# Kernel tuning notes

Hardware: AMD Instinct MI355X
Metric: run time of the kernel (lower is better)

Reference implementation:

```python
import jax, jax.numpy as jnp
import numpy as np

B, T, IN, EH, GH = 256, 512, 128, 512, 512  # batch, time, channels, enc hidden, gen hidden
UPDATE_BIAS = 1.0
CLIP_VAL = 5.0


def setup_inputs() -> dict:
    key = jax.random.key(0)
    ks = jax.random.split(key, 7)
    s = 0.05  # weight scale to keep gates unsaturated
    return {
        "src": jax.random.normal(ks[0], (B, T, IN), jnp.float32),
        "eps": jax.random.normal(ks[1], (B, GH), jnp.float32),  # reparam noise for generator IC
        "enc_Wi": jax.random.normal(ks[2], (3 * EH, IN), jnp.float32) * s,   # torch GRU weight_ih_l0 (r,z,n)
        "enc_Wh": jax.random.normal(ks[3], (3 * EH, EH), jnp.float32) * s,   # torch GRU weight_hh_l0
        "enc2gen_W": jax.random.normal(ks[4], (2 * GH, EH), jnp.float32) * s,  # Linear enc_state -> ic params
        "gen_Wh_ru": jax.random.normal(ks[5], (2 * GH, GH), jnp.float32) * s,  # GruCellModified fc_h_ru
        "gen_W_rhc": jax.random.normal(ks[6], (GH, GH), jnp.float32) * s,      # GruCellModified fc_rh_c
    }


def _forward(src, eps, enc_Wi, enc_Wh, enc2gen_W, gen_Wh_ru, gen_W_rhc):
    b, t, _ = src.shape
    H = enc_Wh.shape[1]
    # ---- encoder: standard GRU (bias=False), batch_first, 1 layer, unidirectional ----
    xW = jnp.einsum('bti,ki->tbk', src, enc_Wi)  # [T,B,3H], input projections hoisted out of scan

    def enc_step(h, xw):
        gh = h @ enc_Wh.T  # [B,3H]
        xr, xz, xn = jnp.split(xw, 3, axis=-1)
        hr, hz, hn = jnp.split(gh, 3, axis=-1)
        r = jax.nn.sigmoid(xr + hr)
        z = jax.nn.sigmoid(xz + hz)
        n = jnp.tanh(xn + r * hn)
        h_new = (1.0 - z) * n + z * h
        return h_new, None

    h0 = jnp.zeros((b, H), src.dtype)
    enc_last, _ = jax.lax.scan(enc_step, h0, xW)  # [B,EH]

    # ---- enc2gen Linear -> generator IC distribution params ----
    ic_params = enc_last @ enc2gen_W.T  # [B, 2*GH]
    mu, lv = jnp.split(ic_params, 2, axis=1)
    ic = mu + jnp.exp(0.5 * lv) * eps  # reparameterized sample, [B,GH]

    # ---- generator: GruCellModified recurrence, input_size=0 (no input term) ----
    def gen_step(h, _):
        ru = h @ gen_Wh_ru.T  # [B,2*GH]
        r, u = jnp.split(ru, 2, axis=-1)
        r = jax.nn.sigmoid(r)
        u = jax.nn.sigmoid(u + UPDATE_BIAS)  # forced update-gate bias
        c = jnp.tanh((r * h) @ gen_W_rhc.T)
        h_new = u * h + (1.0 - u) * c
        return h_new, h_new

    _, gen_hidden = jax.lax.scan(gen_step, ic, None, length=t)  # [T,B,GH]
    gen_out = jnp.clip(gen_hidden.transpose(1, 0, 2), -CLIP_VAL, CLIP_VAL)  # [B,T,GH]
    return gen_out, ic_params


def reference(src, eps, enc_Wi, enc_Wh, enc2gen_W, gen_Wh_ru, gen_W_rhc):
    return _forward(src, eps, enc_Wi, enc_Wh, enc2gen_W, gen_Wh_ru, gen_W_rhc)
```

## Files before the change

### kernel.cpp

```cpp
#include <hip/hip_runtime.h>
#include <hip/hip_bf16.h>
#include <math.h>

#define BB 256
#define TT 512
#define INW 128
#define EH 512
#define GH 512

#define NGRP 16
#define NGB 16
#define MG 16
#define NB 32
#define FLS 16

typedef __attribute__((ext_vector_type(8))) short bf16x8;
typedef __attribute__((ext_vector_type(4))) float f32x4;
typedef __attribute__((ext_vector_type(2))) unsigned long long u64x2;

__device__ __forceinline__ float sigm(float x){ return 1.0f/(1.0f+__expf(-x)); }
__device__ __forceinline__ short f2bf(float x){
    __hip_bfloat16 h = __float2bfloat16(x);
    return *reinterpret_cast<short*>(&h);
}

__device__ __forceinline__ unsigned long long ld_coh64(const unsigned long long* p){
    return __hip_atomic_load(p, __ATOMIC_RELAXED, __HIP_MEMORY_SCOPE_AGENT);
}
__device__ __forceinline__ void st_coh32(unsigned* p, unsigned v){
    __hip_atomic_store(p, v, __ATOMIC_RELAXED, __HIP_MEMORY_SCOPE_AGENT);
}

__device__ __forceinline__ void grp_barrier(unsigned* gf, int ng, unsigned e){
    asm volatile("s_waitcnt vmcnt(0)" ::: "memory");
    __syncthreads();
    if (threadIdx.x == 0) st_coh32(gf + ng*FLS, e);
    if (threadIdx.x < 64) {
        const unsigned* p = gf + (threadIdx.x & (NGB-1)) * FLS;
        long spins = 0;
        for (;;) {
            unsigned v = __hip_atomic_load(p, __ATOMIC_RELAXED, __HIP_MEMORY_SCOPE_AGENT);
            if (__all((int)(v >= e))) break;
            if (++spins > (1L << 20)) break;
        }
    }
    __syncthreads();
}

__device__ __forceinline__ void pack_store_bf(unsigned* dst_even, short bv, int l15){
    unsigned mine = (unsigned short)bv;
    unsigned othr = __shfl_xor(mine, 1);
    if (!(l15 & 1)) st_coh32(dst_even, (othr << 16) | mine);
}

__global__ __launch_bounds__(512, 1) void enc_kernel(
    const float* __restrict__ src,
    const float* __restrict__ Wi,
    const float* __restrict__ Wh,
    short*       __restrict__ hbf,
    float*       __restrict__ hencf,
    unsigned*    __restrict__ flags)
{
    __shared__ __align__(16) char sH[MG*1024];
    __shared__ __align__(16) char sX[MG*256];
    __shared__ float sR[MG*33];
    __shared__ float sZ[MG*33];
    __shared__ float sHfp[MG*33];

    const int bid = blockIdx.x;
    const int g = bid >> 4, ng = bid & 15;
    const int tid = threadIdx.x;
    const int wid = tid >> 6, lane = tid & 63;
    const int l15 = lane & 15, lk = lane >> 4;
    const int j0 = ng * NB;
    const int b0 = g * MG;
    unsigned* gf = flags + g * NGB * FLS;

    bf16x8 whB[16], wxB[4];
    const int gate = wid >> 1, ct = wid & 1;
    const int col = ct*16 + l15;
    if (wid < 6) {
        const float* wrh = Wh + (size_t)(gate*EH + j0 + col) * EH;
        const float* wrx = Wi + (size_t)(gate*EH + j0 + col) * INW;
        #pragma unroll
        for (int kt = 0; kt < 16; ++kt) {
            int ke = kt*32 + lk*8;
            float4 f0 = *(const float4*)(wrh + ke);
            float4 f1 = *(const float4*)(wrh + ke + 4);
            bf16x8 v;
            v[0]=f2bf(f0.x); v[1]=f2bf(f0.y); v[2]=f2bf(f0.z); v[3]=f2bf(f0.w);
            v[4]=f2bf(f1.x); v[5]=f2bf(f1.y); v[6]=f2bf(f1.z); v[7]=f2bf(f1.w);
            whB[kt] = v;
        }
        #pragma unroll
        for (int kt = 0; kt < 4; ++kt) {
            int ke = kt*32 + lk*8;
            float4 f0 = *(const float4*)(wrx + ke);
            float4 f1 = *(const float4*)(wrx + ke + 4);
            bf16x8 v;
            v[0]=f2bf(f0.x); v[1]=f2bf(f0.y); v[2]=f2bf(f0.z); v[3]=f2bf(f0.w);
            v[4]=f2bf(f1.x); v[5]=f2bf(f1.y); v[6]=f2bf(f1.z); v[7]=f2bf(f1.w);
            wxB[kt] = v;
        }
    }
    sHfp[(tid >> 5)*33 + (tid & 31)] = 0.0f;

    for (int t = 0; t < TT; ++t) {
        const short* hsrc = hbf + (size_t)(t & 1) * BB * EH;
        short*       hdst = hbf + (size_t)((t + 1) & 1) * BB * EH;

        #pragma unroll
        for (int i = 0; i < 2; ++i) {
            int c = i*512 + tid;
            int row = c >> 6;
            int kb  = (c & 63) << 4;
            const unsigned long long* gp =
                (const unsigned long long*)((const char*)(hsrc + (size_t)(b0 + row)*EH) + kb);
            unsigned long long v0 = ld_coh64(gp);
            unsigned long long v1 = ld_coh64(gp + 1);
            u64x2 v; v[0] = v0; v[1] = v1;
            *(u64x2*)(sH + row*1024 + (kb ^ ((row & 7) << 4))) = v;
        }
        if (tid < 256) {
            int row = tid >> 4, k = (tid & 15) * 8;
            const float* sp = src + ((size_t)(b0 + row)*TT + t)*INW + k;
            float4 f0 = *(const float4*)sp;
            float4 f1 = *(const float4*)(sp + 4);
            bf16x8 v;
            v[0]=f2bf(f0.x); v[1]=f2bf(f0.y); v[2]=f2bf(f0.z); v[3]=f2bf(f0.w);
            v[4]=f2bf(f1.x); v[5]=f2bf(f1.y); v[6]=f2bf(f1.z); v[7]=f2bf(f1.w);
            *(bf16x8*)(sX + row*256 + ((k*2) ^ ((row & 7) << 4))) = v;
        }
        __syncthreads();

        f32x4 acc0 = {0.f,0.f,0.f,0.f}, acc1 = {0.f,0.f,0.f,0.f};
        f32x4 accx = {0.f,0.f,0.f,0.f};
        if (wid < 6) {
            const int asw = (l15 & 7) << 4;
            const char* hb = sH + l15*1024;
            const char* xb = sX + l15*256;
            #pragma unroll
            for (int kt = 0; kt < 8; ++kt) {
                int kb = kt*64 + lk*16;
                bf16x8 a = *(const bf16x8*)(hb + (kb ^ asw));
                acc0 = __builtin_amdgcn_mfma_f32_16x16x32_bf16(a, whB[kt], acc0, 0, 0, 0);
            }
            #pragma unroll
            for (int kt = 8; kt < 16; ++kt) {
                int kb = kt*64 + lk*16;
                bf16x8 a = *(const bf16x8*)(hb + (kb ^ asw));
                acc1 = __builtin_amdgcn_mfma_f32_16x16x32_bf16(a, whB[kt], acc1, 0, 0, 0);
            }
            #pragma unroll
            for (int kt = 0; kt < 4; ++kt) {
                int kb = kt*64 + lk*16;
                bf16x8 a = *(const bf16x8*)(xb + (kb ^ asw));
                accx = __builtin_amdgcn_mfma_f32_16x16x32_bf16(a, wxB[kt], accx, 0, 0, 0);
            }
        }
        f32x4 acch = acc0 + acc1;
        if (wid < 2) {
            #pragma unroll
            for (int v = 0; v < 4; ++v)
                sR[(lk*4 + v)*33 + col] = sigm(accx[v] + acch[v]);
        } else if (wid < 4) {
            #pragma unroll
            for (int v = 0; v < 4; ++v)
                sZ[(lk*4 + v)*33 + col] = sigm(accx[v] + acch[v]);
        }
        __syncthreads();
        if (wid == 4 || wid == 5) {
            #pragma unroll
            for (int v = 0; v < 4; ++v) {
                int row = lk*4 + v;
                float r  = sR[row*33 + col];
                float z  = sZ[row*33 + col];
                float n  = tanhf(accx[v] + r * acch[v]);
                float hp = sHfp[row*33 + col];
                float hn = (1.f - z)*n + z*hp;
                sHfp[row*33 + col] = hn;
                unsigned* dst = (unsigned*)&hdst[(size_t)(b0 + row)*EH + j0 + ct*16 + (l15 & ~1)];
                pack_store_bf(dst, f2bf(hn), l15);
                if (t == TT - 1) hencf[(size_t)(b0 + row)*EH + j0 + col] = hn;
            }
        }
        grp_barrier(gf, ng, (unsigned)(t + 1));
    }
}

__global__ __launch_bounds__(256) void ic_kernel(
    const float* __restrict__ henc,
    const float* __restrict__ W,
    const float* __restrict__ eps,
    float*       __restrict__ out_icp,
    float*       __restrict__ gh0f,
    short*       __restrict__ gh0b)
{
    __shared__ float hb[EH];
    const int b = blockIdx.x, tid = threadIdx.x;
    for (int k = tid; k < EH; k += 256) hb[k] = henc[(size_t)b*EH + k];
    __syncthreads();

    for (int jj = tid; jj < GH; jj += 256) {
        const float4* wm = (const float4*)(W + (size_t)jj * EH);
        const float4* wl = (const float4*)(W + (size_t)(GH + jj) * EH);
        float am = 0.f, al = 0.f;
        #pragma unroll 4
        for (int k4 = 0; k4 < EH/4; ++k4) {
            float4 h = ((const float4*)hb)[k4];
            float4 a = wm[k4], c = wl[k4];
            am += h.x*a.x + h.y*a.y + h.z*a.z + h.w*a.w;
            al += h.x*c.x + h.y*c.y + h.z*c.z + h.w*c.w;
        }
        out_icp[(size_t)b*2*GH + jj]      = am;
        out_icp[(size_t)b*2*GH + GH + jj] = al;
        float icv = am + __expf(0.5f * al) * eps[(size_t)b*GH + jj];
        gh0f[(size_t)b*GH + jj] = icv;
        gh0b[(size_t)b*GH + jj] = f2bf(icv);
    }
}

__global__ __launch_bounds__(512, 1) void gen_kernel(
    const float* __restrict__ Wru,
    const float* __restrict__ Wc,
    const float* __restrict__ gh0f,
    short*       __restrict__ hbf,
    short*       __restrict__ rhbf,
    float*       __restrict__ out,
    unsigned*    __restrict__ flags)
{
    __shared__ __align__(16) char sH[MG*1024];
    __shared__ float sU[MG*33];
    __shared__ float sHfp[MG*33];

    const int bid = blockIdx.x;
    const int g = bid >> 4, ng = bid & 15;
    const int tid = threadIdx.x;
    const int wid = tid >> 6, lane = tid & 63;
    const int l15 = lane & 15, lk = lane >> 4;
    const int j0 = ng * NB;
    const int b0 = g * MG;
    unsigned* gf = flags + g * NGB * FLS;
    short* rhg = rhbf + (size_t)g * MG * GH;

    bf16x8 wB[16];
    const int gate = wid >> 1, ct = wid & 1;
    const int col = ct*16 + l15;
    if (wid < 6) {
        const float* wr;
        if (gate == 0)      wr = Wru + (size_t)(j0 + col) * GH;
        else if (gate == 1) wr = Wru + (size_t)(GH + j0 + col) * GH;
        else                wr = Wc  + (size_t)(j0 + col) * GH;
        #pragma unroll
        for (int kt = 0; kt < 16; ++kt) {
            int ke = kt*32 + lk*8;
            float4 f0 = *(const float4*)(wr + ke);
            float4 f1 = *(const float4*)(wr + ke + 4);
            bf16x8 v;
            v[0]=f2bf(f0.x); v[1]=f2bf(f0.y); v[2]=f2bf(f0.z); v[3]=f2bf(f0.w);
            v[4]=f2bf(f1.x); v[5]=f2bf(f1.y); v[6]=f2bf(f1.z); v[7]=f2bf(f1.w);
            wB[kt] = v;
        }
    }
    {
        int row = tid >> 5, c = tid & 31;
        sHfp[row*33 + c] = gh0f[(size_t)(b0 + row)*GH + j0 + c];
    }

    for (int t = 0; t < TT; ++t) {
        const short* hsrc = hbf + (size_t)(t & 1) * BB * GH;
        short*       hdst = hbf + (size_t)((t + 1) & 1) * BB * GH;

        #pragma unroll
        for (int i = 0; i < 2; ++i) {
            int c = i*512 + tid;
            int row = c >> 6;
            int kb  = (c & 63) << 4;
            const unsigned long long* gp =
                (const unsigned long long*)((const char*)(hsrc + (size_t)(b0 + row)*GH) + kb);
            unsigned long long v0 = ld_coh64(gp);
            unsigned long long v1 = ld_coh64(gp + 1);
            u64x2 v; v[0] = v0; v[1] = v1;
            *(u64x2*)(sH + row*1024 + (kb ^ ((row & 7) << 4))) = v;
        }
        __syncthreads();

        if (wid < 4) {
            const int asw = (l15 & 7) << 4;
            const char* hb = sH + l15*1024;
            f32x4 acc0 = {0.f,0.f,0.f,0.f}, acc1 = {0.f,0.f,0.f,0.f};
            #pragma unroll
            for (int kt = 0; kt < 8; ++kt) {
                int kb = kt*64 + lk*16;
                bf16x8 a = *(const bf16x8*)(hb + (kb ^ asw));
                acc0 = __builtin_amdgcn_mfma_f32_16x16x32_bf16(a, wB[kt], acc0, 0, 0, 0);
            }
            #pragma unroll
            for (int kt = 8; kt < 16; ++kt) {
                int kb = kt*64 + lk*16;
                bf16x8 a = *(const bf16x8*)(hb + (kb ^ asw));
                acc1 = __builtin_amdgcn_mfma_f32_16x16x32_bf16(a, wB[kt], acc1, 0, 0, 0);
            }
            f32x4 acc = acc0 + acc1;
            if (wid < 2) {
                #pragma unroll
                for (int v = 0; v < 4; ++v) {
                    int row = lk*4 + v;
                    float hp = sHfp[row*33 + col];
                    float rv = sigm(acc[v]);
                    unsigned* dst = (unsigned*)&rhg[(size_t)row*GH + j0 + ct*16 + (l15 & ~1)];
                    pack_store_bf(dst, f2bf(rv * hp), l15);
                }
            } else {
                #pragma unroll
                for (int v = 0; v < 4; ++v)
                    sU[(lk*4 + v)*33 + col] = sigm(acc[v] + 1.0f);
            }
        }
        grp_barrier(gf, ng, (unsigned)(2*t + 1));

        #pragma unroll
        for (int i = 0; i < 2; ++i) {
            int c = i*512 + tid;
            int row = c >> 6;
            int kb  = (c & 63) << 4;
            const unsigned long long* gp =
                (const unsigned long long*)((const char*)(rhg + (size_t)row*GH) + kb);
            unsigned long long v0 = ld_coh64(gp);
            unsigned long long v1 = ld_coh64(gp + 1);
            u64x2 v; v[0] = v0; v[1] = v1;
            *(u64x2*)(sH + row*1024 + (kb ^ ((row & 7) << 4))) = v;
        }
        __syncthreads();

        if (wid == 4 || wid == 5) {
            const int asw = (l15 & 7) << 4;
            const char* hb = sH + l15*1024;
            f32x4 acc0 = {0.f,0.f,0.f,0.f}, acc1 = {0.f,0.f,0.f,0.f};
            #pragma unroll
            for (int kt = 0; kt < 8; ++kt) {
                int kb = kt*64 + lk*16;
                bf16x8 a = *(const bf16x8*)(hb + (kb ^ asw));
                acc0 = __builtin_amdgcn_mfma_f32_16x16x32_bf16(a, wB[kt], acc0, 0, 0, 0);
            }
            #pragma unroll
            for (int kt = 8; kt < 16; ++kt) {
                int kb = kt*64 + lk*16;
                bf16x8 a = *(const bf16x8*)(hb + (kb ^ asw));
                acc1 = __builtin_amdgcn_mfma_f32_16x16x32_bf16(a, wB[kt], acc1, 0, 0, 0);
            }
            f32x4 acc = acc0 + acc1;
            #pragma unroll
            for (int v = 0; v < 4; ++v) {
                int row = lk*4 + v;
                float cv = tanhf(acc[v]);
                float u  = sU[row*33 + col];
                float hp = sHfp[row*33 + col];
                float hn = u*hp + (1.0f - u)*cv;
                sHfp[row*33 + col] = hn;
                unsigned* dst = (unsigned*)&hdst[(size_t)(b0 + row)*GH + j0 + ct*16 + (l15 & ~1)];
                pack_store_bf(dst, f2bf(hn), l15);
                out[((size_t)(b0 + row)*TT + t)*GH + j0 + col] = fminf(fmaxf(hn, -5.0f), 5.0f);
            }
        }
        grp_barrier(gf, ng, (unsigned)(2*t + 2));
    }
}

extern "C" void kernel_launch(void* const* d_in, const int* in_sizes, int n_in,
                              void* d_out, int out_size, void* d_ws, size_t ws_size,
                              hipStream_t stream) {
    (void)in_sizes; (void)n_in; (void)out_size; (void)ws_size;

    const float* src    = (const float*)d_in[0];
    const float* eps    = (const float*)d_in[1];
    const float* enc_Wi = (const float*)d_in[2];
    const float* enc_Wh = (const float*)d_in[3];
    const float* e2g    = (const float*)d_in[4];
    const float* gWru   = (const float*)d_in[5];
    const float* gWc    = (const float*)d_in[6];
    float* out = (float*)d_out;

    char* ws = (char*)d_ws;
    unsigned* encFl = (unsigned*)ws;
    unsigned* genFl = (unsigned*)(ws + 16384);
    float* hencf = (float*)(ws + 32768);
    float* gh0f  = (float*)(ws + 32768 + 512*1024);
    short* encH  = (short*)(ws + 32768 + 1024*1024);
    short* genH  = (short*)(ws + 32768 + 1536*1024);
    short* rhbf  = (short*)(ws + 32768 + 2048*1024);

    hipMemsetAsync(ws, 0, 32768, stream);
    hipMemsetAsync(encH, 0, (size_t)BB*EH*2, stream);

    enc_kernel<<<dim3(256), dim3(512), 0, stream>>>(src, enc_Wi, enc_Wh, encH, hencf, encFl);
    ic_kernel <<<dim3(256), dim3(256), 0, stream>>>(hencf, e2g, eps,
                                                    out + (size_t)BB*TT*GH, gh0f, genH);
    gen_kernel<<<dim3(256), dim3(512), 0, stream>>>(gWru, gWc, gh0f, genH, rhbf, out,
                                                    genFl);
}
```

Before: 4.905 ms.

## Split each block's batch tile into two half-groups and ping-pong their recurrence steps

Each workgroup now owns two independent 8-row batch sub-groups with separate flag sets and double-buffered shared tiles. It alternates compute between them, so the group-barrier wait and global staging loads of one half overlap with the MFMA work of the other. Hidden-state loads for the next half are issued right after polling and written to LDS later, which hides load latency behind compute. In exchange, half of each 16-row MFMA tile is wasted, there are twice as many flag polls per step, and the synchronisation pattern is more complex and fragile.

```diff
diff --git a/kernel.cpp b/kernel.cpp
--- a/kernel.cpp
+++ b/kernel.cpp
@@ -8,9 +8,8 @@
 #define EH 512
 #define GH 512
 
-#define NGRP 16
 #define NGB 16
-#define MG 16
+#define MGH 8
 #define NB 32
 #define FLS 16
 
@@ -30,15 +29,23 @@
 __device__ __forceinline__ void st_coh32(unsigned* p, unsigned v){
     __hip_atomic_store(p, v, __ATOMIC_RELAXED, __HIP_MEMORY_SCOPE_AGENT);
 }
-
-__device__ __forceinline__ void grp_barrier(unsigned* gf, int ng, unsigned e){
-    asm volatile("s_waitcnt vmcnt(0)" ::: "memory");
-    __syncthreads();
-    if (threadIdx.x == 0) st_coh32(gf + ng*FLS, e);
-    if (threadIdx.x < 64) {
-        const unsigned* p = gf + (threadIdx.x & (NGB-1)) * FLS;
+__device__ __forceinline__ void wait_vm0(){ asm volatile("s_waitcnt vmcnt(0)" ::: "memory"); }
+
+struct Stg { unsigned long long q0, q1; };
+__device__ __forceinline__ Stg stage_issue(const short* rowbase, int kb){
+    const unsigned long long* gp = (const unsigned long long*)((const char*)rowbase + kb);
+    Stg s; s.q0 = ld_coh64(gp); s.q1 = ld_coh64(gp + 1); return s;
+}
+__device__ __forceinline__ void stage_write(char* sbuf, int row, int kb, Stg s){
+    u64x2 v; v[0] = s.q0; v[1] = s.q1;
+    *(u64x2*)(sbuf + row*1024 + (kb ^ (row << 4))) = v;
+}
+
+__device__ __forceinline__ void poll16(const unsigned* fl, unsigned e){
+    if (threadIdx.x < 64){
+        const unsigned* p = fl + (threadIdx.x & (NGB-1)) * FLS;
         long spins = 0;
-        for (;;) {
+        for(;;){
             unsigned v = __hip_atomic_load(p, __ATOMIC_RELAXED, __HIP_MEMORY_SCOPE_AGENT);
             if (__all((int)(v >= e))) break;
             if (++spins > (1L << 20)) break;
@@ -47,10 +54,143 @@
     __syncthreads();
 }
 
-__device__ __forceinline__ void pack_store_bf(unsigned* dst_even, short bv, int l15){
-    unsigned mine = (unsigned short)bv;
-    unsigned othr = __shfl_xor(mine, 1);
-    if (!(l15 & 1)) st_coh32(dst_even, (othr << 16) | mine);
+__device__ __forceinline__ void xwrite(char* sX, int row, int kf, float4 f){
+    short4 v;
+    v.x = f2bf(f.x); v.y = f2bf(f.y); v.z = f2bf(f.z); v.w = f2bf(f.w);
+    *(short4*)(sX + row*256 + ((kf*2) ^ (row << 4))) = v;
+}
+
+__device__ __forceinline__ void enc_compute(
+    const char* sH, const char* sX, float* sR, float* sZ, float* sHfp,
+    const bf16x8* whB, const bf16x8* wxB,
+    short* hdst, float* hencf, const int b0, const int j0,
+    const int wid, const int l15, const int lk, const int ct, const int col,
+    const bool last)
+{
+    f32x4 acc0 = {0.f,0.f,0.f,0.f}, acc1 = {0.f,0.f,0.f,0.f}, accx = {0.f,0.f,0.f,0.f};
+    if (wid < 6){
+        const int r8 = l15 & 7;
+        const int asw = r8 << 4;
+        const char* hb = sH + r8*1024;
+        const char* xb = sX + r8*256;
+        #pragma unroll
+        for (int kt = 0; kt < 8; ++kt){ int kb = kt*64 + lk*16;
+            bf16x8 a = *(const bf16x8*)(hb + (kb ^ asw));
+            acc0 = __builtin_amdgcn_mfma_f32_16x16x32_bf16(a, whB[kt], acc0, 0, 0, 0); }
+        #pragma unroll
+        for (int kt = 8; kt < 16; ++kt){ int kb = kt*64 + lk*16;
+            bf16x8 a = *(const bf16x8*)(hb + (kb ^ asw));
+            acc1 = __builtin_amdgcn_mfma_f32_16x16x32_bf16(a, whB[kt], acc1, 0, 0, 0); }
+        #pragma unroll
+        for (int kt = 0; kt < 4; ++kt){ int kb = kt*64 + lk*16;
+            bf16x8 a = *(const bf16x8*)(xb + (kb ^ asw));
+            accx = __builtin_amdgcn_mfma_f32_16x16x32_bf16(a, wxB[kt], accx, 0, 0, 0); }
+    }
+    f32x4 acch = acc0 + acc1;
+    if (wid < 2){
+        #pragma unroll
+        for (int v = 0; v < 4; ++v){ int row = lk*4 + v;
+            if (row < MGH) sR[row*33 + col] = sigm(accx[v] + acch[v]); }
+    } else if (wid < 4){
+        #pragma unroll
+        for (int v = 0; v < 4; ++v){ int row = lk*4 + v;
+            if (row < MGH) sZ[row*33 + col] = sigm(accx[v] + acch[v]); }
+    }
+    __syncthreads();
+    if (wid == 4 || wid == 5){
+        #pragma unroll
+        for (int v = 0; v < 4; ++v){ int row = lk*4 + v;
+            if (row < MGH){
+                float r  = sR[row*33 + col];
+                float z  = sZ[row*33 + col];
+                float n  = tanhf(accx[v] + r * acch[v]);
+                float hp = sHfp[row*33 + col];
+                float hn = (1.f - z)*n + z*hp;
+                sHfp[row*33 + col] = hn;
+                unsigned mine = (unsigned short)f2bf(hn);
+                unsigned oth  = __shfl_xor(mine, 1);
+                if (!(l15 & 1))
+                    st_coh32((unsigned*)&hdst[(size_t)(b0 + row)*EH + j0 + ct*16 + (l15 & ~1)],
+                             (oth << 16) | mine);
+                if (last) hencf[(size_t)(b0 + row)*EH + j0 + col] = hn;
+            }
+        }
+    }
+}
+
+__device__ __forceinline__ void gen_ph1(
+    const char* sH, float* sU, const float* sHfp, const bf16x8* wB,
+    short* rhg, const int j0, const int wid, const int l15, const int lk,
+    const int ct, const int col)
+{
+    if (wid < 4){
+        const int r8 = l15 & 7, asw = r8 << 4;
+        const char* hb = sH + r8*1024;
+        f32x4 a0 = {0.f,0.f,0.f,0.f}, a1 = {0.f,0.f,0.f,0.f};
+        #pragma unroll
+        for (int kt = 0; kt < 8; ++kt){ int kb = kt*64 + lk*16;
+            bf16x8 a = *(const bf16x8*)(hb + (kb ^ asw));
+            a0 = __builtin_amdgcn_mfma_f32_16x16x32_bf16(a, wB[kt], a0, 0, 0, 0); }
+        #pragma unroll
+        for (int kt = 8; kt < 16; ++kt){ int kb = kt*64 + lk*16;
+            bf16x8 a = *(const bf16x8*)(hb + (kb ^ asw));
+            a1 = __builtin_amdgcn_mfma_f32_16x16x32_bf16(a, wB[kt], a1, 0, 0, 0); }
+        f32x4 acc = a0 + a1;
+        if (wid < 2){
+            #pragma unroll
+            for (int v = 0; v < 4; ++v){ int row = lk*4 + v;
+                if (row < MGH){
+                    float hp = sHfp[row*33 + col];
+                    float rv = sigm(acc[v]);
+                    unsigned mine = (unsigned short)f2bf(rv * hp);
+                    unsigned oth  = __shfl_xor(mine, 1);
+                    if (!(l15 & 1))
+                        st_coh32((unsigned*)&rhg[(size_t)row*GH + j0 + ct*16 + (l15 & ~1)],
+                                 (oth << 16) | mine);
+                }}
+        } else {
+            #pragma unroll
+            for (int v = 0; v < 4; ++v){ int row = lk*4 + v;
+                if (row < MGH) sU[row*33 + col] = sigm(acc[v] + 1.0f); }
+        }
+    }
+}
+
+__device__ __forceinline__ void gen_ph2(
+    const char* sH , const float* sU, float* sHfp, const bf16x8* wB,
+    short* hdst, const int b0, const int j0, const int wid, const int l15,
+    const int lk, const int ct, const int col, float* hvv)
+{
+    if (wid == 4 || wid == 5){
+        const int r8 = l15 & 7, asw = r8 << 4;
+        const char* hb = sH + r8*1024;
+        f32x4 a0 = {0.f,0.f,0.f,0.f}, a1 = {0.f,0.f,0.f,0.f};
+        #pragma unroll
+        for (int kt = 0; kt < 8; ++kt){ int kb = kt*64 + lk*16;
+            bf16x8 a = *(const bf16x8*)(hb + (kb ^ asw));
+            a0 = __builtin_amdgcn_mfma_f32_16x16x32_bf16(a, wB[kt], a0, 0, 0, 0); }
+        #pragma unroll
+        for (int kt = 8; kt < 16; ++kt){ int kb = kt*64 + lk*16;
+            bf16x8 a = *(const bf16x8*)(hb + (kb ^ asw));
+            a1 = __builtin_amdgcn_mfma_f32_16x16x32_bf16(a, wB[kt], a1, 0, 0, 0); }
+        f32x4 acc = a0 + a1;
+        #pragma unroll
+        for (int v = 0; v < 4; ++v){ int row = lk*4 + v;
+            if (row < MGH){
+                float cv = tanhf(acc[v]);
+                float u  = sU[row*33 + col];
+                float hp = sHfp[row*33 + col];
+                float hn = u*hp + (1.0f - u)*cv;
+                sHfp[row*33 + col] = hn;
+                hvv[v] = hn;
+                unsigned mine = (unsigned short)f2bf(hn);
+                unsigned oth  = __shfl_xor(mine, 1);
+                if (!(l15 & 1))
+                    st_coh32((unsigned*)&hdst[(size_t)(b0 + row)*GH + j0 + ct*16 + (l15 & ~1)],
+                             (oth << 16) | mine);
+            }
+        }
+    }
 }
 
 __global__ __launch_bounds__(512, 1) void enc_kernel(
@@ -61,29 +201,32 @@
     float*       __restrict__ hencf,
     unsigned*    __restrict__ flags)
 {
-    __shared__ __align__(16) char sH[MG*1024];
-    __shared__ __align__(16) char sX[MG*256];
-    __shared__ float sR[MG*33];
-    __shared__ float sZ[MG*33];
-    __shared__ float sHfp[MG*33];
+    __shared__ __align__(16) char sHA[MGH*1024];
+    __shared__ __align__(16) char sHB[MGH*1024];
+    __shared__ __align__(16) char sXA[MGH*256];
+    __shared__ __align__(16) char sXB[MGH*256];
+    __shared__ float sR[MGH*33], sZ[MGH*33];
+    __shared__ float sHfpA[MGH*33], sHfpB[MGH*33];
 
     const int bid = blockIdx.x;
-    const int g = bid >> 4, ng = bid & 15;
+    const int pr = bid >> 4, ng = bid & 15;
     const int tid = threadIdx.x;
     const int wid = tid >> 6, lane = tid & 63;
     const int l15 = lane & 15, lk = lane >> 4;
     const int j0 = ng * NB;
-    const int b0 = g * MG;
-    unsigned* gf = flags + g * NGB * FLS;
-
-    bf16x8 whB[16], wxB[4];
+    const int b0A = pr * 16, b0B = pr * 16 + 8;
+    unsigned* flA = flags + (size_t)((pr << 1) | 0) * (NGB * FLS);
+    unsigned* flB = flags + (size_t)((pr << 1) | 1) * (NGB * FLS);
+
     const int gate = wid >> 1, ct = wid & 1;
     const int col = ct*16 + l15;
-    if (wid < 6) {
+
+    bf16x8 whB[16], wxB[4];
+    if (wid < 6){
         const float* wrh = Wh + (size_t)(gate*EH + j0 + col) * EH;
         const float* wrx = Wi + (size_t)(gate*EH + j0 + col) * INW;
         #pragma unroll
-        for (int kt = 0; kt < 16; ++kt) {
+        for (int kt = 0; kt < 16; ++kt){
             int ke = kt*32 + lk*8;
             float4 f0 = *(const float4*)(wrh + ke);
             float4 f1 = *(const float4*)(wrh + ke + 4);
@@ -93,7 +236,7 @@
             whB[kt] = v;
         }
         #pragma unroll
-        for (int kt = 0; kt < 4; ++kt) {
+        for (int kt = 0; kt < 4; ++kt){
             int ke = kt*32 + lk*8;
             float4 f0 = *(const float4*)(wrx + ke);
             float4 f1 = *(const float4*)(wrx + ke + 4);
@@ -103,88 +246,56 @@
             wxB[kt] = v;
         }
     }
-    sHfp[(tid >> 5)*33 + (tid & 31)] = 0.0f;
-
-    for (int t = 0; t < TT; ++t) {
-        const short* hsrc = hbf + (size_t)(t & 1) * BB * EH;
-        short*       hdst = hbf + (size_t)((t + 1) & 1) * BB * EH;
-
-        #pragma unroll
-        for (int i = 0; i < 2; ++i) {
-            int c = i*512 + tid;
-            int row = c >> 6;
-            int kb  = (c & 63) << 4;
-            const unsigned long long* gp =
-                (const unsigned long long*)((const char*)(hsrc + (size_t)(b0 + row)*EH) + kb);
-            unsigned long long v0 = ld_coh64(gp);
-            unsigned long long v1 = ld_coh64(gp + 1);
-            u64x2 v; v[0] = v0; v[1] = v1;
-            *(u64x2*)(sH + row*1024 + (kb ^ ((row & 7) << 4))) = v;
-        }
-        if (tid < 256) {
-            int row = tid >> 4, k = (tid & 15) * 8;
-            const float* sp = src + ((size_t)(b0 + row)*TT + t)*INW + k;
-            float4 f0 = *(const float4*)sp;
-            float4 f1 = *(const float4*)(sp + 4);
-            bf16x8 v;
-            v[0]=f2bf(f0.x); v[1]=f2bf(f0.y); v[2]=f2bf(f0.z); v[3]=f2bf(f0.w);
-            v[4]=f2bf(f1.x); v[5]=f2bf(f1.y); v[6]=f2bf(f1.z); v[7]=f2bf(f1.w);
-            *(bf16x8*)(sX + row*256 + ((k*2) ^ ((row & 7) << 4))) = v;
-        }
-        __syncthreads();
-
-        f32x4 acc0 = {0.f,0.f,0.f,0.f}, acc1 = {0.f,0.f,0.f,0.f};
-        f32x4 accx = {0.f,0.f,0.f,0.f};
-        if (wid < 6) {
-            const int asw = (l15 & 7) << 4;
-            const char* hb = sH + l15*1024;
-            const char* xb = sX + l15*256;
-            #pragma unroll
-            for (int kt = 0; kt < 8; ++kt) {
-                int kb = kt*64 + lk*16;
-                bf16x8 a = *(const bf16x8*)(hb + (kb ^ asw));
-                acc0 = __builtin_amdgcn_mfma_f32_16x16x32_bf16(a, whB[kt], acc0, 0, 0, 0);
-            }
-            #pragma unroll
-            for (int kt = 8; kt < 16; ++kt) {
-                int kb = kt*64 + lk*16;
-                bf16x8 a = *(const bf16x8*)(hb + (kb ^ asw));
-                acc1 = __builtin_amdgcn_mfma_f32_16x16x32_bf16(a, whB[kt], acc1, 0, 0, 0);
-            }
-            #pragma unroll
-            for (int kt = 0; kt < 4; ++kt) {
-                int kb = kt*64 + lk*16;
-                bf16x8 a = *(const bf16x8*)(xb + (kb ^ asw));
-                accx = __builtin_amdgcn_mfma_f32_16x16x32_bf16(a, wxB[kt], accx, 0, 0, 0);
-            }
-        }
-        f32x4 acch = acc0 + acc1;
-        if (wid < 2) {
-            #pragma unroll
-            for (int v = 0; v < 4; ++v)
-                sR[(lk*4 + v)*33 + col] = sigm(accx[v] + acch[v]);
-        } else if (wid < 4) {
-            #pragma unroll
-            for (int v = 0; v < 4; ++v)
-                sZ[(lk*4 + v)*33 + col] = sigm(accx[v] + acch[v]);
-        }
-        __syncthreads();
-        if (wid == 4 || wid == 5) {
-            #pragma unroll
-            for (int v = 0; v < 4; ++v) {
-                int row = lk*4 + v;
-                float r  = sR[row*33 + col];
-                float z  = sZ[row*33 + col];
-                float n  = tanhf(accx[v] + r * acch[v]);
-                float hp = sHfp[row*33 + col];
-                float hn = (1.f - z)*n + z*hp;
-                sHfp[row*33 + col] = hn;
-                unsigned* dst = (unsigned*)&hdst[(size_t)(b0 + row)*EH + j0 + ct*16 + (l15 & ~1)];
-                pack_store_bf(dst, f2bf(hn), l15);
-                if (t == TT - 1) hencf[(size_t)(b0 + row)*EH + j0 + col] = hn;
-            }
-        }
-        grp_barrier(gf, ng, (unsigned)(t + 1));
+
+    const int srow = tid >> 6;
+    const int skb  = (tid & 63) << 4;
+    const int xrow = tid >> 5;
+    const int xkf  = (tid & 31) * 4;
+
+    if (tid < MGH*NB){ int row = tid >> 5, c = tid & 31;
+        sHfpA[row*33 + c] = 0.f; sHfpB[row*33 + c] = 0.f; }
+    { u64x2 z; z[0]=0; z[1]=0;
+      *(u64x2*)(sHA + srow*1024 + (skb ^ (srow<<4))) = z;
+      *(u64x2*)(sHB + srow*1024 + (skb ^ (srow<<4))) = z; }
+    float4 xrA, xrB;
+    if (tid < 256){
+        xrA = *(const float4*)(src + ((size_t)(b0A + xrow)*TT + 0)*INW + xkf);
+        xrB = *(const float4*)(src + ((size_t)(b0B + xrow)*TT + 0)*INW + xkf);
+        xwrite(sXA, xrow, xkf, xrA);
+    }
+    Stg ldA, ldB; ldB.q0 = 0; ldB.q1 = 0;
+    __syncthreads();
+
+    for (int t = 0; t < TT; ++t){
+        short* hdst = hbf + (size_t)((t + 1) & 1) * BB * EH;
+
+        enc_compute(sHA, sXA, sR, sZ, sHfpA, whB, wxB, hdst, hencf, b0A, j0,
+                    wid, l15, lk, ct, col, t == TT-1);
+        wait_vm0(); __syncthreads();
+        if (tid == 0) st_coh32(flA + ng*FLS, (unsigned)(t + 1));
+        stage_write(sHB, srow, skb, ldB);
+        if (tid < 256) xwrite(sXB, xrow, xkf, xrB);
+        poll16(flA, (unsigned)(t + 1));
+        if (t < TT-1){
+            ldA = stage_issue(hdst + (size_t)(b0A + srow)*EH, skb);
+            if (tid < 256)
+                xrA = *(const float4*)(src + ((size_t)(b0A + xrow)*TT + (t+1))*INW + xkf);
+        }
+
+        enc_compute(sHB, sXB, sR, sZ, sHfpB, whB, wxB, hdst, hencf, b0B, j0,
+                    wid, l15, lk, ct, col, t == TT-1);
+        wait_vm0(); __syncthreads();
+        if (tid == 0) st_coh32(flB + ng*FLS, (unsigned)(t + 1));
+        if (t < TT-1){
+            stage_write(sHA, srow, skb, ldA);
+            if (tid < 256) xwrite(sXA, xrow, xkf, xrA);
+        }
+        poll16(flB, (unsigned)(t + 1));
+        if (t < TT-1){
+            ldB = stage_issue(hdst + (size_t)(b0B + srow)*EH, skb);
+            if (tid < 256)
+                xrB = *(const float4*)(src + ((size_t)(b0B + xrow)*TT + (t+1))*INW + xkf);
+        }
     }
 }
 
@@ -201,12 +312,12 @@
     for (int k = tid; k < EH; k += 256) hb[k] = henc[(size_t)b*EH + k];
     __syncthreads();
 
-    for (int jj = tid; jj < GH; jj += 256) {
+    for (int jj = tid; jj < GH; jj += 256){
         const float4* wm = (const float4*)(W + (size_t)jj * EH);
         const float4* wl = (const float4*)(W + (size_t)(GH + jj) * EH);
         float am = 0.f, al = 0.f;
         #pragma unroll 4
-        for (int k4 = 0; k4 < EH/4; ++k4) {
+        for (int k4 = 0; k4 < EH/4; ++k4){
             float4 h = ((const float4*)hb)[k4];
             float4 a = wm[k4], c = wl[k4];
             am += h.x*a.x + h.y*a.y + h.z*a.z + h.w*a.w;
@@ -229,30 +340,36 @@
     float*       __restrict__ out,
     unsigned*    __restrict__ flags)
 {
-    __shared__ __align__(16) char sH[MG*1024];
-    __shared__ float sU[MG*33];
-    __shared__ float sHfp[MG*33];
+    __shared__ __align__(16) char sHA[MGH*1024];
+    __shared__ __align__(16) char sHB[MGH*1024];
+    __shared__ float sUA[MGH*33], sUB[MGH*33];
+    __shared__ float sHfpA[MGH*33], sHfpB[MGH*33];
 
     const int bid = blockIdx.x;
-    const int g = bid >> 4, ng = bid & 15;
+    const int pr = bid >> 4, ng = bid & 15;
     const int tid = threadIdx.x;
     const int wid = tid >> 6, lane = tid & 63;
     const int l15 = lane & 15, lk = lane >> 4;
     const int j0 = ng * NB;
-    const int b0 = g * MG;
-    unsigned* gf = flags + g * NGB * FLS;
-    short* rhg = rhbf + (size_t)g * MG * GH;
-
-    bf16x8 wB[16];
+    const int b0A = pr * 16, b0B = pr * 16 + 8;
+    unsigned* flrA = flags + (size_t)(pr*4 + 0) * (NGB*FLS);
+    unsigned* flhA = flags + (size_t)(pr*4 + 1) * (NGB*FLS);
+    unsigned* flrB = flags + (size_t)(pr*4 + 2) * (NGB*FLS);
+    unsigned* flhB = flags + (size_t)(pr*4 + 3) * (NGB*FLS);
+    short* rhgA = rhbf + (size_t)(pr*2 + 0) * MGH * GH;
+    short* rhgB = rhbf + (size_t)(pr*2 + 1) * MGH * GH;
+
     const int gate = wid >> 1, ct = wid & 1;
     const int col = ct*16 + l15;
-    if (wid < 6) {
+
+    bf16x8 wB[16];
+    if (wid < 6){
         const float* wr;
         if (gate == 0)      wr = Wru + (size_t)(j0 + col) * GH;
         else if (gate == 1) wr = Wru + (size_t)(GH + j0 + col) * GH;
         else                wr = Wc  + (size_t)(j0 + col) * GH;
         #pragma unroll
-        for (int kt = 0; kt < 16; ++kt) {
+        for (int kt = 0; kt < 16; ++kt){
             int ke = kt*32 + lk*8;
             float4 f0 = *(const float4*)(wr + ke);
             float4 f1 = *(const float4*)(wr + ke + 4);
@@ -262,108 +379,64 @@
             wB[kt] = v;
         }
     }
-    {
-        int row = tid >> 5, c = tid & 31;
-        sHfp[row*33 + c] = gh0f[(size_t)(b0 + row)*GH + j0 + c];
-    }
-
-    for (int t = 0; t < TT; ++t) {
-        const short* hsrc = hbf + (size_t)(t & 1) * BB * GH;
-        short*       hdst = hbf + (size_t)((t + 1) & 1) * BB * GH;
-
-        #pragma unroll
-        for (int i = 0; i < 2; ++i) {
-            int c = i*512 + tid;
-            int row = c >> 6;
-            int kb  = (c & 63) << 4;
-            const unsigned long long* gp =
-                (const unsigned long long*)((const char*)(hsrc + (size_t)(b0 + row)*GH) + kb);
-            unsigned long long v0 = ld_coh64(gp);
-            unsigned long long v1 = ld_coh64(gp + 1);
-            u64x2 v; v[0] = v0; v[1] = v1;
-            *(u64x2*)(sH + row*1024 + (kb ^ ((row & 7) << 4))) = v;
-        }
-        __syncthreads();
-
-        if (wid < 4) {
-            const int asw = (l15 & 7) << 4;
-            const char* hb = sH + l15*1024;
-            f32x4 acc0 = {0.f,0.f,0.f,0.f}, acc1 = {0.f,0.f,0.f,0.f};
+
+    const int srow = tid >> 6;
+    const int skb  = (tid & 63) << 4;
+
+    if (tid < MGH*NB){ int row = tid >> 5, c = tid & 31;
+        sHfpA[row*33 + c] = gh0f[(size_t)(b0A + row)*GH + j0 + c];
+        sHfpB[row*33 + c] = gh0f[(size_t)(b0B + row)*GH + j0 + c]; }
+    Stg ldA = stage_issue(hbf + (size_t)(b0A + srow)*GH, skb);
+    Stg ldB = stage_issue(hbf + (size_t)(b0B + srow)*GH, skb);
+    stage_write(sHA, srow, skb, ldA);
+    __syncthreads();
+
+    for (int t = 0; t < TT; ++t){
+        short* slotN = hbf + (size_t)((t + 1) & 1) * BB * GH;
+
+        gen_ph1(sHA, sUA, sHfpA, wB, rhgA, j0, wid, l15, lk, ct, col);
+        wait_vm0(); __syncthreads();
+        if (tid == 0) st_coh32(flrA + ng*FLS, (unsigned)(t + 1));
+        stage_write(sHB, srow, skb, ldB);
+        poll16(flrA, (unsigned)(t + 1));
+        Stg ldrA = stage_issue(rhgA + (size_t)srow*GH, skb);
+
+        gen_ph1(sHB, sUB, sHfpB, wB, rhgB, j0, wid, l15, lk, ct, col);
+        wait_vm0(); __syncthreads();
+        if (tid == 0) st_coh32(flrB + ng*FLS, (unsigned)(t + 1));
+        stage_write(sHA, srow, skb, ldrA);
+        poll16(flrB, (unsigned)(t + 1));
+        Stg ldrB = stage_issue(rhgB + (size_t)srow*GH, skb);
+
+        float hvA[4];
+        gen_ph2(sHA, sUA, sHfpA, wB, slotN, b0A, j0, wid, l15, lk, ct, col, hvA);
+        wait_vm0(); __syncthreads();
+        if (tid == 0) st_coh32(flhA + ng*FLS, (unsigned)(t + 1));
+        if (wid == 4 || wid == 5){
             #pragma unroll
-            for (int kt = 0; kt < 8; ++kt) {
-                int kb = kt*64 + lk*16;
-                bf16x8 a = *(const bf16x8*)(hb + (kb ^ asw));
-                acc0 = __builtin_amdgcn_mfma_f32_16x16x32_bf16(a, wB[kt], acc0, 0, 0, 0);
-            }
+            for (int v = 0; v < 4; ++v){ int row = lk*4 + v;
+                if (row < MGH)
+                    out[((size_t)(b0A + row)*TT + t)*GH + j0 + col] =
+                        fminf(fmaxf(hvA[v], -5.0f), 5.0f); }
+        }
+        stage_write(sHB, srow, skb, ldrB);
+        poll16(flhA, (unsigned)(t + 1));
+        if (t < TT-1) ldA = stage_issue(slotN + (size_t)(b0A + srow)*GH, skb);
+
+        float hvB[4];
+        gen_ph2(sHB, sUB, sHfpB, wB, slotN, b0B, j0, wid, l15, lk, ct, col, hvB);
+        wait_vm0(); __syncthreads();
+        if (tid == 0) st_coh32(flhB + ng*FLS, (unsigned)(t + 1));
+        if (wid == 4 || wid == 5){
             #pragma unroll
-            for (int kt = 8; kt < 16; ++kt) {
-                int kb = kt*64 + lk*16;
-                bf16x8 a = *(const bf16x8*)(hb + (kb ^ asw));
-                acc1 = __builtin_amdgcn_mfma_f32_16x16x32_bf16(a, wB[kt], acc1, 0, 0, 0);
-            }
-            f32x4 acc = acc0 + acc1;
-            if (wid < 2) {
-                #pragma unroll
-                for (int v = 0; v < 4; ++v) {
-                    int row = lk*4 + v;
-                    float hp = sHfp[row*33 + col];
-                    float rv = sigm(acc[v]);
-                    unsigned* dst = (unsigned*)&rhg[(size_t)row*GH + j0 + ct*16 + (l15 & ~1)];
-                    pack_store_bf(dst, f2bf(rv * hp), l15);
-                }
-            } else {
-                #pragma unroll
-                for (int v = 0; v < 4; ++v)
-                    sU[(lk*4 + v)*33 + col] = sigm(acc[v] + 1.0f);
-            }
-        }
-        grp_barrier(gf, ng, (unsigned)(2*t + 1));
-
-        #pragma unroll
-        for (int i = 0; i < 2; ++i) {
-            int c = i*512 + tid;
-            int row = c >> 6;
-            int kb  = (c & 63) << 4;
-            const unsigned long long* gp =
-                (const unsigned long long*)((const char*)(rhg + (size_t)row*GH) + kb);
-            unsigned long long v0 = ld_coh64(gp);
-            unsigned long long v1 = ld_coh64(gp + 1);
-            u64x2 v; v[0] = v0; v[1] = v1;
-            *(u64x2*)(sH + row*1024 + (kb ^ ((row & 7) << 4))) = v;
-        }
-        __syncthreads();
-
-        if (wid == 4 || wid == 5) {
-            const int asw = (l15 & 7) << 4;
-            const char* hb = sH + l15*1024;
-            f32x4 acc0 = {0.f,0.f,0.f,0.f}, acc1 = {0.f,0.f,0.f,0.f};
-            #pragma unroll
-            for (int kt = 0; kt < 8; ++kt) {
-                int kb = kt*64 + lk*16;
-                bf16x8 a = *(const bf16x8*)(hb + (kb ^ asw));
-                acc0 = __builtin_amdgcn_mfma_f32_16x16x32_bf16(a, wB[kt], acc0, 0, 0, 0);
-            }
-            #pragma unroll
-            for (int kt = 8; kt < 16; ++kt) {
-                int kb = kt*64 + lk*16;
-                bf16x8 a = *(const bf16x8*)(hb + (kb ^ asw));
-                acc1 = __builtin_amdgcn_mfma_f32_16x16x32_bf16(a, wB[kt], acc1, 0, 0, 0);
-            }
-            f32x4 acc = acc0 + acc1;
-            #pragma unroll
-            for (int v = 0; v < 4; ++v) {
-                int row = lk*4 + v;
-                float cv = tanhf(acc[v]);
-                float u  = sU[row*33 + col];
-                float hp = sHfp[row*33 + col];
-                float hn = u*hp + (1.0f - u)*cv;
-                sHfp[row*33 + col] = hn;
-                unsigned* dst = (unsigned*)&hdst[(size_t)(b0 + row)*GH + j0 + ct*16 + (l15 & ~1)];
-                pack_store_bf(dst, f2bf(hn), l15);
-                out[((size_t)(b0 + row)*TT + t)*GH + j0 + col] = fminf(fmaxf(hn, -5.0f), 5.0f);
-            }
-        }
-        grp_barrier(gf, ng, (unsigned)(2*t + 2));
+            for (int v = 0; v < 4; ++v){ int row = lk*4 + v;
+                if (row < MGH)
+                    out[((size_t)(b0B + row)*TT + t)*GH + j0 + col] =
+                        fminf(fmaxf(hvB[v], -5.0f), 5.0f); }
+        }
+        if (t < TT-1) stage_write(sHA, srow, skb, ldA);
+        poll16(flhB, (unsigned)(t + 1));
+        if (t < TT-1) ldB = stage_issue(slotN + (size_t)(b0B + srow)*GH, skb);
     }
 }
 
@@ -383,14 +456,14 @@
 
     char* ws = (char*)d_ws;
     unsigned* encFl = (unsigned*)ws;
-    unsigned* genFl = (unsigned*)(ws + 16384);
-    float* hencf = (float*)(ws + 32768);
-    float* gh0f  = (float*)(ws + 32768 + 512*1024);
-    short* encH  = (short*)(ws + 32768 + 1024*1024);
-    short* genH  = (short*)(ws + 32768 + 1536*1024);
-    short* rhbf  = (short*)(ws + 32768 + 2048*1024);
-
-    hipMemsetAsync(ws, 0, 32768, stream);
+    unsigned* genFl = (unsigned*)(ws + 32768);
+    float* hencf = (float*)(ws + 131072);
+    float* gh0f  = (float*)(ws + 131072 + 512*1024);
+    short* encH  = (short*)(ws + 131072 + 1024*1024);
+    short* genH  = (short*)(ws + 131072 + 1536*1024);
+    short* rhbf  = (short*)(ws + 131072 + 2048*1024);
+
+    hipMemsetAsync(ws, 0, 98304, stream);
     hipMemsetAsync(encH, 0, (size_t)BB*EH*2, stream);
 
     enc_kernel<<<dim3(256), dim3(512), 0, stream>>>(src, enc_Wi, enc_Wh, encH, hencf, encFl);
```

Result: slower. 7.258 ms (+48.0%).
